# Kernel optimization log

Measured on AMD Instinct MI355X. Metric: run time of the kernel, lower is better.

## Reference

```python
import jax, jax.numpy as jnp
import numpy as np

B, H, S = 16, 1024, 2048

def setup_inputs() -> dict:
    key = jax.random.key(0)
    kf, kz, ki = jax.random.split(key, 3)
    f = jax.random.uniform(kf, (B, H, S), dtype=jnp.float32)
    z = jax.random.normal(kz, (B, H, S), dtype=jnp.float32)
    i = jax.random.uniform(ki, (B, H, S), dtype=jnp.float32)
    return {"f": f, "z": z, "i": i}

def reference(f, z, i):
    # Inputs are [batch, hidden, seq]; recurrence runs over seq:
    #   h_t = f_t * h_{t-1} + i_t * z_t, h_{-1} = 0
    fs = jnp.transpose(f, (2, 0, 1))  # [S, B, H]
    xs = jnp.transpose(i * z, (2, 0, 1))  # [S, B, H]

    def step(h_prev, fx):
        f_t, x_t = fx
        h_t = f_t * h_prev + x_t
        return h_t, h_t

    h0 = jnp.zeros(fs.shape[1:], dtype=fs.dtype)
    _, hs = jax.lax.scan(step, h0, (fs, xs))  # [S, B, H]
    return jnp.transpose(hs, (1, 2, 0))  # [B, H, S]
```

## Files before the change

kernel.cpp:

```cpp
#include <hip/hip_runtime.h>


constexpr int S_LEN = 2048;
constexpr int TPB   = 512;

template<int CTRL, int RM>
__device__ __forceinline__ float dpp_mov_f(float old_v, float src) {
    return __int_as_float(__builtin_amdgcn_update_dpp(
        __float_as_int(old_v), __float_as_int(src), CTRL, RM, 0xf, false));
}

template<int CTRL, int RM>
__device__ __forceinline__ void scan_step(float& a, float& b) {
    const float a_up = dpp_mov_f<CTRL, RM>(1.0f, a);
    const float b_up = dpp_mov_f<CTRL, RM>(0.0f, b);
    b = __builtin_fmaf(a, b_up, b);
    a = a * a_up;
}

__global__ __launch_bounds__(TPB) void ifo_scan_kernel(
    const float* __restrict__ f,
    const float* __restrict__ z,
    const float* __restrict__ iin,
    float* __restrict__ out)
{
    const size_t base = (size_t)blockIdx.x * S_LEN;
    const int t    = threadIdx.x;
    const int lane = t & 63;
    const int wave = t >> 6;

    const float4 ff = reinterpret_cast<const float4*>(f   + base)[t];
    const float4 zz = reinterpret_cast<const float4*>(z   + base)[t];
    const float4 ii = reinterpret_cast<const float4*>(iin + base)[t];

    float4 xx;
    xx.x = ii.x * zz.x;
    xx.y = ii.y * zz.y;
    xx.z = ii.z * zz.z;
    xx.w = ii.w * zz.w;

    float A = ff.x, B = xx.x;
    A = ff.y * A;  B = ff.y * B + xx.y;
    A = ff.z * A;  B = ff.z * B + xx.z;
    A = ff.w * A;  B = ff.w * B + xx.w;

    float a = A, b = B;
    scan_step<0x111, 0xf>(a, b);
    scan_step<0x112, 0xf>(a, b);
    scan_step<0x114, 0xf>(a, b);
    scan_step<0x118, 0xf>(a, b);
    scan_step<0x142, 0xa>(a, b);
    scan_step<0x143, 0xc>(a, b);

    __shared__ float wa[8], wb[8];
    if (lane == 63) { wa[wave] = a; wb[wave] = b; }
    __syncthreads();

    float pb = 0.0f;
    for (int w = 0; w < wave; ++w) {
        pb = wa[w] * pb + wb[w];
    }

    const float ea = dpp_mov_f<0x138, 0xf>(1.0f, a);
    const float eb = dpp_mov_f<0x138, 0xf>(0.0f, b);

    float h = ea * pb + eb;

    float4 oo;
    h = ff.x * h + xx.x;  oo.x = h;
    h = ff.y * h + xx.y;  oo.y = h;
    h = ff.z * h + xx.z;  oo.z = h;
    h = ff.w * h + xx.w;  oo.w = h;
    reinterpret_cast<float4*>(out + base)[t] = oo;
}

extern "C" void kernel_launch(void* const* d_in, const int* in_sizes, int n_in,
                              void* d_out, int out_size, void* d_ws, size_t ws_size,
                              hipStream_t stream) {
    const float* f = (const float*)d_in[0];
    const float* z = (const float*)d_in[1];
    const float* i = (const float*)d_in[2];
    float* out = (float*)d_out;

    const int rows = out_size / S_LEN;
    ifo_scan_kernel<<<rows, TPB, 0, stream>>>(f, z, i, out);
}
```

Measured before the change: 378.8 us.

## Process eight rows per block with software-prefetched loads and double-buffered LDS

Each block now handles eight rows instead of one, prefetching the next row's f/z/i float4 loads while scanning the current row. Cross-wave carries use double-buffered shared arrays so only one barrier is needed per row. The carry combine becomes a branchless predicated FMA chain over vector LDS reads, and outputs use nontemporal stores. Together these aim to hide memory latency and cut launch and barrier overhead. The cost is fewer blocks (2048 rather than 16384) and more registers per thread.

```diff
diff --git a/kernel.cpp b/kernel.cpp
--- a/kernel.cpp
+++ b/kernel.cpp
@@ -1,8 +1,11 @@
 #include <hip/hip_runtime.h>
 
 
+typedef float f32x4 __attribute__((ext_vector_type(4)));
+
 constexpr int S_LEN = 2048;
 constexpr int TPB   = 512;
+constexpr int RPB   = 8;
 
 template<int CTRL, int RM>
 __device__ __forceinline__ float dpp_mov_f(float old_v, float src) {
@@ -18,21 +21,11 @@
     a = a * a_up;
 }
 
-__global__ __launch_bounds__(TPB) void ifo_scan_kernel(
-    const float* __restrict__ f,
-    const float* __restrict__ z,
-    const float* __restrict__ iin,
-    float* __restrict__ out)
+__device__ __forceinline__ void process_row(
+    const float4 ff, const float4 zz, const float4 ii,
+    float* __restrict__ outp, const int t, const int lane, const int wave,
+    float (&wa)[2][8], float (&wb)[2][8], const int parity)
 {
-    const size_t base = (size_t)blockIdx.x * S_LEN;
-    const int t    = threadIdx.x;
-    const int lane = t & 63;
-    const int wave = t >> 6;
-
-    const float4 ff = reinterpret_cast<const float4*>(f   + base)[t];
-    const float4 zz = reinterpret_cast<const float4*>(z   + base)[t];
-    const float4 ii = reinterpret_cast<const float4*>(iin + base)[t];
-
     float4 xx;
     xx.x = ii.x * zz.x;
     xx.y = ii.y * zz.y;
@@ -52,26 +45,77 @@
     scan_step<0x142, 0xa>(a, b);
     scan_step<0x143, 0xc>(a, b);
 
-    __shared__ float wa[8], wb[8];
-    if (lane == 63) { wa[wave] = a; wb[wave] = b; }
+    if (lane == 63) { wa[parity][wave] = a; wb[parity][wave] = b; }
     __syncthreads();
 
+    const f32x4 wa0 = *reinterpret_cast<const f32x4*>(&wa[parity][0]);
+    const f32x4 wa1 = *reinterpret_cast<const f32x4*>(&wa[parity][4]);
+    const f32x4 wb0 = *reinterpret_cast<const f32x4*>(&wb[parity][0]);
+    const f32x4 wb1 = *reinterpret_cast<const f32x4*>(&wb[parity][4]);
+
     float pb = 0.0f;
-    for (int w = 0; w < wave; ++w) {
-        pb = wa[w] * pb + wb[w];
-    }
+    float tmp;
+    tmp = __builtin_fmaf(wa0.x, pb, wb0.x); pb = (0 < wave) ? tmp : pb;
+    tmp = __builtin_fmaf(wa0.y, pb, wb0.y); pb = (1 < wave) ? tmp : pb;
+    tmp = __builtin_fmaf(wa0.z, pb, wb0.z); pb = (2 < wave) ? tmp : pb;
+    tmp = __builtin_fmaf(wa0.w, pb, wb0.w); pb = (3 < wave) ? tmp : pb;
+    tmp = __builtin_fmaf(wa1.x, pb, wb1.x); pb = (4 < wave) ? tmp : pb;
+    tmp = __builtin_fmaf(wa1.y, pb, wb1.y); pb = (5 < wave) ? tmp : pb;
+    tmp = __builtin_fmaf(wa1.z, pb, wb1.z); pb = (6 < wave) ? tmp : pb;
 
     const float ea = dpp_mov_f<0x138, 0xf>(1.0f, a);
     const float eb = dpp_mov_f<0x138, 0xf>(0.0f, b);
 
-    float h = ea * pb + eb;
+    float h = __builtin_fmaf(ea, pb, eb);
 
-    float4 oo;
+    f32x4 oo;
     h = ff.x * h + xx.x;  oo.x = h;
     h = ff.y * h + xx.y;  oo.y = h;
     h = ff.z * h + xx.z;  oo.z = h;
     h = ff.w * h + xx.w;  oo.w = h;
-    reinterpret_cast<float4*>(out + base)[t] = oo;
+    __builtin_nontemporal_store(oo, reinterpret_cast<f32x4*>(outp) + t);
+}
+
+__global__ __launch_bounds__(TPB) void ifo_scan_kernel(
+    const float* __restrict__ f,
+    const float* __restrict__ z,
+    const float* __restrict__ iin,
+    float* __restrict__ out,
+    int n_rows)
+{
+    const int t    = threadIdx.x;
+    const int lane = t & 63;
+    const int wave = t >> 6;
+    const size_t row0 = (size_t)blockIdx.x * RPB;
+    if (row0 >= (size_t)n_rows) return;
+
+    __shared__ __align__(16) float wa[2][8], wb[2][8];
+
+    const float4* __restrict__ F = reinterpret_cast<const float4*>(f);
+    const float4* __restrict__ Z = reinterpret_cast<const float4*>(z);
+    const float4* __restrict__ I = reinterpret_cast<const float4*>(iin);
+    constexpr int V4 = S_LEN / 4;
+
+    const size_t v0 = row0 * V4 + t;
+
+    float4 fA = F[v0], zA = Z[v0], iA = I[v0];
+
+    #pragma unroll
+    for (int r = 0; r < RPB; r += 2) {
+        const size_t i1 = v0 + (size_t)(r + 1) * V4;
+        float4 fB = F[i1], zB = Z[i1], iB = I[i1];
+
+        process_row(fA, zA, iA, out + (row0 + r) * S_LEN,
+                    t, lane, wave, wa, wb, 0);
+
+        if (r + 2 < RPB) {
+            const size_t i2 = v0 + (size_t)(r + 2) * V4;
+            fA = F[i2]; zA = Z[i2]; iA = I[i2];
+        }
+
+        process_row(fB, zB, iB, out + (row0 + r + 1) * S_LEN,
+                    t, lane, wave, wa, wb, 1);
+    }
 }
 
 extern "C" void kernel_launch(void* const* d_in, const int* in_sizes, int n_in,
@@ -83,5 +127,6 @@
     float* out = (float*)d_out;
 
     const int rows = out_size / S_LEN;
-    ifo_scan_kernel<<<rows, TPB, 0, stream>>>(f, z, i, out);
+    const int grid = (rows + RPB - 1) / RPB;
+    ifo_scan_kernel<<<grid, TPB, 0, stream>>>(f, z, i, out, rows);
 }
```

Measured after the change: 396.9 us. 4.8% more time.
